# Optimization experiments

Measured on AMD Instinct MI355X. Metric: run time of the kernel, lower is better.

Reference implementation:

```python
import jax, jax.numpy as jnp
import numpy as np

RGB_W = (0.2989, 0.587, 0.114)
EPS = 1e-8  # guard only; original divides without eps


def _saliency_map(img):
    """Faithful jax port of SaliencyMap: gray -> uint8 -> cv2.Sobel(ksize=3,
    BORDER_REFLECT_101) -> magnitude -> per-image min-max normalize.
    img: [B, C, H, W] float in [0,1]. Returns [B, 1, H, W] float32.
    """
    B, C, H, W = img.shape
    if C == 3:
        gray = RGB_W[0] * img[:, 0] + RGB_W[1] * img[:, 1] + RGB_W[2] * img[:, 2]
    else:
        gray = img[:, 0]
    # (gray*255).astype(np.uint8): truncating cast, then cv2 promotes to float
    q = (gray * 255.0).astype(jnp.uint8).astype(jnp.float32)  # [B,H,W]
    # cv2 default border: BORDER_REFLECT_101 == jnp.pad mode 'reflect'
    p = jnp.pad(q, ((0, 0), (1, 1), (1, 1)), mode='reflect')  # [B,H+2,W+2]
    # Sobel x (correlation with [[-1,0,1],[-2,0,2],[-1,0,1]])
    gx = (p[:, :-2, 2:] + 2.0 * p[:, 1:-1, 2:] + p[:, 2:, 2:]
          - p[:, :-2, :-2] - 2.0 * p[:, 1:-1, :-2] - p[:, 2:, :-2])
    # Sobel y (transpose kernel)
    gy = (p[:, 2:, :-2] + 2.0 * p[:, 2:, 1:-1] + p[:, 2:, 2:]
          - p[:, :-2, :-2] - 2.0 * p[:, :-2, 1:-1] - p[:, :-2, 2:])
    mag = jnp.sqrt(gx * gx + gy * gy)  # [B,H,W]
    mn = jnp.min(mag, axis=(1, 2), keepdims=True)
    mx = jnp.max(mag, axis=(1, 2), keepdims=True)
    norm = (mag - mn) / jnp.maximum(mx - mn, EPS)  # cv2 NORM_MINMAX to [0,1]
    return norm[:, None]  # [B,1,H,W]


def setup_inputs() -> dict:
    key = jax.random.key(0)
    k1, k2, k3 = jax.random.split(key, 3)
    shape = (16, 3, 512, 512)
    return {
        "img_vis": jax.random.uniform(k1, shape, dtype=jnp.float32),
        "img_ir": jax.random.uniform(k2, shape, dtype=jnp.float32),
        "img_fusion": jax.random.uniform(k3, shape, dtype=jnp.float32),
    }


def reference(img_vis, img_ir, img_fusion):
    s_vis = _saliency_map(img_vis)  # [B,1,H,W]
    s_ir = _saliency_map(img_ir)
    denom = s_vis + s_ir + EPS  # eps guard against 0/0 (see notes)
    w_vis = s_vis / denom
    w_ir = s_ir / denom
    img_sal = w_vis * img_vis + w_ir * img_ir  # broadcasts over channels
    loss = jnp.mean(jnp.abs(img_sal - img_fusion))  # F.l1_loss (mean)
    return loss
```

## Files before the change

kernel.cpp:

```cpp
#include <hip/hip_runtime.h>
#include <hip/hip_bf16.h>
#include <stdint.h>

#define H 512
#define W 512
#define HW (H * W)
#define NSTRIP 128

__device__ __forceinline__ int refl(int i, int n) {
    return i < 0 ? -i : (i >= n ? 2 * n - 2 - i : i);
}

__device__ __forceinline__ uint2 gray8(float4 ra, float4 rb, float4 ga, float4 gb,
                                       float4 ba, float4 bb) {
    uint32_t t0 = (uint32_t)((0.2989f * ra.x + 0.587f * ga.x + 0.114f * ba.x) * 255.0f);
    uint32_t t1 = (uint32_t)((0.2989f * ra.y + 0.587f * ga.y + 0.114f * ba.y) * 255.0f);
    uint32_t t2 = (uint32_t)((0.2989f * ra.z + 0.587f * ga.z + 0.114f * ba.z) * 255.0f);
    uint32_t t3 = (uint32_t)((0.2989f * ra.w + 0.587f * ga.w + 0.114f * ba.w) * 255.0f);
    uint32_t t4 = (uint32_t)((0.2989f * rb.x + 0.587f * gb.x + 0.114f * bb.x) * 255.0f);
    uint32_t t5 = (uint32_t)((0.2989f * rb.y + 0.587f * gb.y + 0.114f * bb.y) * 255.0f);
    uint32_t t6 = (uint32_t)((0.2989f * rb.z + 0.587f * gb.z + 0.114f * bb.z) * 255.0f);
    uint32_t t7 = (uint32_t)((0.2989f * rb.w + 0.587f * gb.w + 0.114f * bb.w) * 255.0f);
    uint2 o;
    o.x = t0 | (t1 << 8) | (t2 << 16) | (t3 << 24);
    o.y = t4 | (t5 << 8) | (t6 << 16) | (t7 << 24);
    return o;
}

__global__ __launch_bounds__(256) void k_gray(const float* __restrict__ vis,
                                              const float* __restrict__ ir,
                                              uint8_t* __restrict__ qvis,
                                              uint8_t* __restrict__ qir, int B) {
    int lane = threadIdx.x & 63;
    int gwave = blockIdx.x * 4 + (threadIdx.x >> 6);
    int per_src = B * 256;
    int src = gwave >= per_src;
    int rem = src ? gwave - per_src : gwave;
    int b  = rem >> 8;
    int y0 = (rem & 255) * 2;

    const float4* p4 = (const float4*)((src ? ir : vis) + (size_t)b * 3 * HW);
    uint8_t* q = (src ? qir : qvis) + (size_t)b * HW;

    int o0 = y0 * (W / 4) + lane * 2;
    int o1 = o0 + (W / 4);
    float4 r0a = p4[o0],                 r0b = p4[o0 + 1];
    float4 g0a = p4[o0 + HW / 4],        g0b = p4[o0 + 1 + HW / 4];
    float4 b0a = p4[o0 + 2 * (HW / 4)],  b0b = p4[o0 + 1 + 2 * (HW / 4)];
    float4 r1a = p4[o1],                 r1b = p4[o1 + 1];
    float4 g1a = p4[o1 + HW / 4],        g1b = p4[o1 + 1 + HW / 4];
    float4 b1a = p4[o1 + 2 * (HW / 4)],  b1b = p4[o1 + 1 + 2 * (HW / 4)];

    uint2 q0 = gray8(r0a, r0b, g0a, g0b, b0a, b0b);
    uint2 q1 = gray8(r1a, r1b, g1a, g1b, b1a, b1b);
    *(uint2*)(q + (size_t)y0 * W + lane * 8)       = q0;
    *(uint2*)(q + (size_t)(y0 + 1) * W + lane * 8) = q1;
}

__device__ __forceinline__ void row_cols(uint2 v, int lane, float* __restrict__ c) {
    uint32_t lx = __shfl_up(v.y, 1);
    uint32_t rx = __shfl_down(v.x, 1);
    uint32_t lb = (lane == 0)  ? ((v.x >> 8) & 0xffu)  : (lx >> 24);
    uint32_t rb = (lane == 63) ? ((v.y >> 16) & 0xffu) : (rx & 0xffu);
    c[0] = (float)lb;
    c[1] = (float)(v.x & 0xffu);
    c[2] = (float)((v.x >> 8) & 0xffu);
    c[3] = (float)((v.x >> 16) & 0xffu);
    c[4] = (float)(v.x >> 24);
    c[5] = (float)(v.y & 0xffu);
    c[6] = (float)((v.y >> 8) & 0xffu);
    c[7] = (float)((v.y >> 16) & 0xffu);
    c[8] = (float)(v.y >> 24);
    c[9] = (float)rb;
}

__device__ __forceinline__ void sobel_row8(const uint8_t* __restrict__ q, int y, int lane,
                                           float* __restrict__ mag) {
    const uint2* rm = (const uint2*)(q + (size_t)refl(y - 1, H) * W);
    const uint2* r0 = (const uint2*)(q + (size_t)y * W);
    const uint2* rp = (const uint2*)(q + (size_t)refl(y + 1, H) * W);
    uint2 vm = rm[lane], v0 = r0[lane], vp = rp[lane];
    float c0[10], c1[10], c2[10];
    row_cols(vm, lane, c0);
    row_cols(v0, lane, c1);
    row_cols(vp, lane, c2);
    float sx[10], sy[10];
    #pragma unroll
    for (int j = 0; j < 10; ++j) {
        sx[j] = c0[j] + 2.0f * c1[j] + c2[j];
        sy[j] = c2[j] - c0[j];
    }
    #pragma unroll
    for (int k = 0; k < 8; ++k) {
        float gx = sx[k + 2] - sx[k];
        float gy = sy[k] + 2.0f * sy[k + 1] + sy[k + 2];
        mag[k] = sqrtf(gx * gx + gy * gy);
    }
}

__global__ __launch_bounds__(256) void k_mm(const uint8_t* __restrict__ qvis,
                                            const uint8_t* __restrict__ qir,
                                            float* __restrict__ pm, int B) {
    int lane = threadIdx.x & 63;
    int gwave = blockIdx.x * 4 + (threadIdx.x >> 6);
    int per_src = B * NSTRIP;
    int src = gwave >= per_src;
    int rem = src ? gwave - per_src : gwave;
    int b     = rem >> 7;
    int strip = rem & 127;
    int y0 = strip * 4;
    const uint8_t* q = (src ? qir : qvis) + (size_t)b * HW;

    float mn = INFINITY, mx = 0.0f;
    #pragma unroll
    for (int r = 0; r < 4; ++r) {
        float mag[8];
        sobel_row8(q, y0 + r, lane, mag);
        #pragma unroll
        for (int k = 0; k < 8; ++k) {
            mn = fminf(mn, mag[k]);
            mx = fmaxf(mx, mag[k]);
        }
    }
    #pragma unroll
    for (int o = 32; o > 0; o >>= 1) {
        mn = fminf(mn, __shfl_down(mn, o));
        mx = fmaxf(mx, __shfl_down(mx, o));
    }
    if (lane == 0) {
        float* o = pm + ((size_t)(src * B + b) * NSTRIP + strip) * 2;
        o[0] = mn;
        o[1] = mx;
    }
}

__global__ __launch_bounds__(256) void k_loss(const float* __restrict__ vis,
                                              const float* __restrict__ ir,
                                              const float* __restrict__ fus,
                                              const uint8_t* __restrict__ qvis,
                                              const uint8_t* __restrict__ qir,
                                              const float* __restrict__ pm,
                                              float* __restrict__ partial, int B) {
    int w = threadIdx.x >> 6, lane = threadIdx.x & 63;
    int b = blockIdx.x >> 6;
    int y0 = (blockIdx.x & 63) * 8;

    __shared__ float sred[4];
    {
        int src = w >> 1, qsel = w & 1;
        const float* base = pm + (size_t)(src * B + b) * NSTRIP * 2;
        float v0 = base[lane * 2 + qsel];
        float v1 = base[(lane + 64) * 2 + qsel];
        float v = qsel ? fmaxf(v0, v1) : fminf(v0, v1);
        if (qsel == 0) {
            #pragma unroll
            for (int o = 32; o > 0; o >>= 1) v = fminf(v, __shfl_down(v, o));
        } else {
            #pragma unroll
            for (int o = 32; o > 0; o >>= 1) v = fmaxf(v, __shfl_down(v, o));
        }
        if (lane == 0) sred[w] = v;
    }
    __syncthreads();
    float mn_v = sred[0], mx_v = sred[1], mn_i = sred[2], mx_i = sred[3];
    float inv_v = 1.0f / fmaxf(mx_v - mn_v, 1e-8f);
    float inv_i = 1.0f / fmaxf(mx_i - mn_i, 1e-8f);

    float acc = 0.0f;
    #pragma unroll
    for (int rr = 0; rr < 2; ++rr) {
        int y = y0 + w + rr * 4;
        float mv[8], mi[8];
        sobel_row8(qvis + (size_t)b * HW, y, lane, mv);
        sobel_row8(qir  + (size_t)b * HW, y, lane, mi);

        float wv[8], wi[8];
        #pragma unroll
        for (int k = 0; k < 8; ++k) {
            float sv = (mv[k] - mn_v) * inv_v;
            float si = (mi[k] - mn_i) * inv_i;
            float den = sv + si + 1e-8f;
            float rden = 1.0f / den;
            wv[k] = sv * rden;
            wi[k] = si * rden;
        }

        int i = y * W + lane * 8;
        #pragma unroll
        for (int ch = 0; ch < 3; ++ch) {
            size_t e4 = ((((size_t)b * 3 + ch) * HW) + i) >> 2;
            const float4* v4 = (const float4*)vis;
            const float4* r4 = (const float4*)ir;
            const float4* f4 = (const float4*)fus;
            float4 va = v4[e4], vb = v4[e4 + 1];
            float4 ra = r4[e4], rb = r4[e4 + 1];
            float4 fa = f4[e4], fb = f4[e4 + 1];
            acc += fabsf(wv[0] * va.x + wi[0] * ra.x - fa.x);
            acc += fabsf(wv[1] * va.y + wi[1] * ra.y - fa.y);
            acc += fabsf(wv[2] * va.z + wi[2] * ra.z - fa.z);
            acc += fabsf(wv[3] * va.w + wi[3] * ra.w - fa.w);
            acc += fabsf(wv[4] * vb.x + wi[4] * rb.x - fb.x);
            acc += fabsf(wv[5] * vb.y + wi[5] * rb.y - fb.y);
            acc += fabsf(wv[6] * vb.z + wi[6] * rb.z - fb.z);
            acc += fabsf(wv[7] * vb.w + wi[7] * rb.w - fb.w);
        }
    }

    #pragma unroll
    for (int o = 32; o > 0; o >>= 1) acc += __shfl_down(acc, o);
    __shared__ float ssum[4];
    if (lane == 0) ssum[w] = acc;
    __syncthreads();
    if (threadIdx.x == 0) partial[blockIdx.x] = ssum[0] + ssum[1] + ssum[2] + ssum[3];
}

__global__ void k_final(const float* __restrict__ partial, int n, float* __restrict__ out,
                        long long N) {
    double s = 0.0;
    for (int i = threadIdx.x; i < n; i += 256) s += (double)partial[i];
    __shared__ double sm[256];
    sm[threadIdx.x] = s;
    __syncthreads();
    for (int k = 128; k > 0; k >>= 1) {
        if (threadIdx.x < k) sm[threadIdx.x] += sm[threadIdx.x + k];
        __syncthreads();
    }
    if (threadIdx.x == 0) out[0] = (float)(sm[0] / (double)N);
}

extern "C" void kernel_launch(void* const* d_in, const int* in_sizes, int n_in,
                              void* d_out, int out_size, void* d_ws, size_t ws_size,
                              hipStream_t stream) {
    const float* vis = (const float*)d_in[0];
    const float* ir  = (const float*)d_in[1];
    const float* fus = (const float*)d_in[2];
    int B = in_sizes[0] / (3 * HW);

    uint8_t* qvis = (uint8_t*)d_ws;
    uint8_t* qir  = qvis + (size_t)B * HW;
    float* pm      = (float*)(qir + (size_t)B * HW);
    float* partial = pm + (size_t)2 * B * NSTRIP * 2;
    float* out = (float*)d_out;

    int nblk_gray = 2 * B * 256 / 4;
    k_gray<<<nblk_gray, 256, 0, stream>>>(vis, ir, qvis, qir, B);

    int nblk_mm = 2 * B * NSTRIP / 4;
    k_mm<<<nblk_mm, 256, 0, stream>>>(qvis, qir, pm, B);

    int nblk_loss = B * (H / 8);
    k_loss<<<nblk_loss, 256, 0, stream>>>(vis, ir, fus, qvis, qir, pm, partial, B);

    k_final<<<1, 256, 0, stream>>>(partial, nblk_loss, out, (long long)B * 3 * HW);
}
```

Baseline: 58.65 us.

## Fuse grayscale quantization into Sobel kernels and drop uint8 intermediate

```diff
diff --git a/kernel.cpp b/kernel.cpp
--- a/kernel.cpp
+++ b/kernel.cpp
@@ -11,84 +11,46 @@
     return i < 0 ? -i : (i >= n ? 2 * n - 2 - i : i);
 }
 
-__device__ __forceinline__ uint2 gray8(float4 ra, float4 rb, float4 ga, float4 gb,
-                                       float4 ba, float4 bb) {
-    uint32_t t0 = (uint32_t)((0.2989f * ra.x + 0.587f * ga.x + 0.114f * ba.x) * 255.0f);
-    uint32_t t1 = (uint32_t)((0.2989f * ra.y + 0.587f * ga.y + 0.114f * ba.y) * 255.0f);
-    uint32_t t2 = (uint32_t)((0.2989f * ra.z + 0.587f * ga.z + 0.114f * ba.z) * 255.0f);
-    uint32_t t3 = (uint32_t)((0.2989f * ra.w + 0.587f * ga.w + 0.114f * ba.w) * 255.0f);
-    uint32_t t4 = (uint32_t)((0.2989f * rb.x + 0.587f * gb.x + 0.114f * bb.x) * 255.0f);
-    uint32_t t5 = (uint32_t)((0.2989f * rb.y + 0.587f * gb.y + 0.114f * bb.y) * 255.0f);
-    uint32_t t6 = (uint32_t)((0.2989f * rb.z + 0.587f * gb.z + 0.114f * bb.z) * 255.0f);
-    uint32_t t7 = (uint32_t)((0.2989f * rb.w + 0.587f * gb.w + 0.114f * bb.w) * 255.0f);
-    uint2 o;
-    o.x = t0 | (t1 << 8) | (t2 << 16) | (t3 << 24);
-    o.y = t4 | (t5 << 8) | (t6 << 16) | (t7 << 24);
-    return o;
-}
-
-__global__ __launch_bounds__(256) void k_gray(const float* __restrict__ vis,
-                                              const float* __restrict__ ir,
-                                              uint8_t* __restrict__ qvis,
-                                              uint8_t* __restrict__ qir, int B) {
-    int lane = threadIdx.x & 63;
-    int gwave = blockIdx.x * 4 + (threadIdx.x >> 6);
-    int per_src = B * 256;
-    int src = gwave >= per_src;
-    int rem = src ? gwave - per_src : gwave;
-    int b  = rem >> 8;
-    int y0 = (rem & 255) * 2;
-
-    const float4* p4 = (const float4*)((src ? ir : vis) + (size_t)b * 3 * HW);
-    uint8_t* q = (src ? qir : qvis) + (size_t)b * HW;
-
-    int o0 = y0 * (W / 4) + lane * 2;
-    int o1 = o0 + (W / 4);
-    float4 r0a = p4[o0],                 r0b = p4[o0 + 1];
-    float4 g0a = p4[o0 + HW / 4],        g0b = p4[o0 + 1 + HW / 4];
-    float4 b0a = p4[o0 + 2 * (HW / 4)],  b0b = p4[o0 + 1 + 2 * (HW / 4)];
-    float4 r1a = p4[o1],                 r1b = p4[o1 + 1];
-    float4 g1a = p4[o1 + HW / 4],        g1b = p4[o1 + 1 + HW / 4];
-    float4 b1a = p4[o1 + 2 * (HW / 4)],  b1b = p4[o1 + 1 + 2 * (HW / 4)];
-
-    uint2 q0 = gray8(r0a, r0b, g0a, g0b, b0a, b0b);
-    uint2 q1 = gray8(r1a, r1b, g1a, g1b, b1a, b1b);
-    *(uint2*)(q + (size_t)y0 * W + lane * 8)       = q0;
-    *(uint2*)(q + (size_t)(y0 + 1) * W + lane * 8) = q1;
-}
-
-__device__ __forceinline__ void row_cols(uint2 v, int lane, float* __restrict__ c) {
-    uint32_t lx = __shfl_up(v.y, 1);
-    uint32_t rx = __shfl_down(v.x, 1);
-    uint32_t lb = (lane == 0)  ? ((v.x >> 8) & 0xffu)  : (lx >> 24);
-    uint32_t rb = (lane == 63) ? ((v.y >> 16) & 0xffu) : (rx & 0xffu);
-    c[0] = (float)lb;
-    c[1] = (float)(v.x & 0xffu);
-    c[2] = (float)((v.x >> 8) & 0xffu);
-    c[3] = (float)((v.x >> 16) & 0xffu);
-    c[4] = (float)(v.x >> 24);
-    c[5] = (float)(v.y & 0xffu);
-    c[6] = (float)((v.y >> 8) & 0xffu);
-    c[7] = (float)((v.y >> 16) & 0xffu);
-    c[8] = (float)(v.y >> 24);
-    c[9] = (float)rb;
-}
-
-__device__ __forceinline__ void sobel_row8(const uint8_t* __restrict__ q, int y, int lane,
-                                           float* __restrict__ mag) {
-    const uint2* rm = (const uint2*)(q + (size_t)refl(y - 1, H) * W);
-    const uint2* r0 = (const uint2*)(q + (size_t)y * W);
-    const uint2* rp = (const uint2*)(q + (size_t)refl(y + 1, H) * W);
-    uint2 vm = rm[lane], v0 = r0[lane], vp = rp[lane];
-    float c0[10], c1[10], c2[10];
-    row_cols(vm, lane, c0);
-    row_cols(v0, lane, c1);
-    row_cols(vp, lane, c2);
+__device__ __forceinline__ void gray8f(float4 ra, float4 rb, float4 ga, float4 gb,
+                                       float4 ba, float4 bb, float* __restrict__ g) {
+    g[0] = floorf((0.2989f * ra.x + 0.587f * ga.x + 0.114f * ba.x) * 255.0f);
+    g[1] = floorf((0.2989f * ra.y + 0.587f * ga.y + 0.114f * ba.y) * 255.0f);
+    g[2] = floorf((0.2989f * ra.z + 0.587f * ga.z + 0.114f * ba.z) * 255.0f);
+    g[3] = floorf((0.2989f * ra.w + 0.587f * ga.w + 0.114f * ba.w) * 255.0f);
+    g[4] = floorf((0.2989f * rb.x + 0.587f * gb.x + 0.114f * bb.x) * 255.0f);
+    g[5] = floorf((0.2989f * rb.y + 0.587f * gb.y + 0.114f * bb.y) * 255.0f);
+    g[6] = floorf((0.2989f * rb.z + 0.587f * gb.z + 0.114f * bb.z) * 255.0f);
+    g[7] = floorf((0.2989f * rb.w + 0.587f * gb.w + 0.114f * bb.w) * 255.0f);
+}
+
+__device__ __forceinline__ void grayrow(const float4* __restrict__ p4, int row, int lane,
+                                        float* __restrict__ g) {
+    int o = row * (W / 4) + lane * 2;
+    float4 ra = p4[o],                 rb = p4[o + 1];
+    float4 ga = p4[o + HW / 4],        gb = p4[o + 1 + HW / 4];
+    float4 ba = p4[o + 2 * (HW / 4)],  bb = p4[o + 1 + 2 * (HW / 4)];
+    gray8f(ra, rb, ga, gb, ba, bb, g);
+}
+
+__device__ __forceinline__ void win10(const float* __restrict__ g, int lane,
+                                      float* __restrict__ h) {
+    #pragma unroll
+    for (int j = 0; j < 8; ++j) h[j + 1] = g[j];
+    float up = __shfl_up(g[7], 1);
+    float dn = __shfl_down(g[0], 1);
+    h[0] = (lane == 0)  ? g[1] : up;
+    h[9] = (lane == 63) ? g[6] : dn;
+}
+
+__device__ __forceinline__ void sobel8(const float* __restrict__ hm,
+                                       const float* __restrict__ h0,
+                                       const float* __restrict__ hp,
+                                       float* __restrict__ mag) {
     float sx[10], sy[10];
     #pragma unroll
     for (int j = 0; j < 10; ++j) {
-        sx[j] = c0[j] + 2.0f * c1[j] + c2[j];
-        sy[j] = c2[j] - c0[j];
+        sx[j] = hm[j] + 2.0f * h0[j] + hp[j];
+        sy[j] = hp[j] - hm[j];
     }
     #pragma unroll
     for (int k = 0; k < 8; ++k) {
@@ -98,24 +60,39 @@
     }
 }
 
-__global__ __launch_bounds__(256) void k_mm(const uint8_t* __restrict__ qvis,
-                                            const uint8_t* __restrict__ qir,
+__device__ __forceinline__ void sobel_rgb(const float4* __restrict__ p4, int y, int lane,
+                                          float* __restrict__ mag) {
+    float gm[8], g0[8], gp[8];
+    grayrow(p4, refl(y - 1, H), lane, gm);
+    grayrow(p4, y,              lane, g0);
+    grayrow(p4, refl(y + 1, H), lane, gp);
+    float hm[10], h0[10], hp[10];
+    win10(gm, lane, hm);
+    win10(g0, lane, h0);
+    win10(gp, lane, hp);
+    sobel8(hm, h0, hp, mag);
+}
+
+__global__ __launch_bounds__(256) void k_mm(const float* __restrict__ vis,
+                                            const float* __restrict__ ir,
                                             float* __restrict__ pm, int B) {
     int lane = threadIdx.x & 63;
-    int gwave = blockIdx.x * 4 + (threadIdx.x >> 6);
+    int nwg = gridDim.x;
+    int bid = (blockIdx.x & 7) * (nwg >> 3) + (blockIdx.x >> 3);
+    int gwave = bid * 4 + (threadIdx.x >> 6);
     int per_src = B * NSTRIP;
     int src = gwave >= per_src;
     int rem = src ? gwave - per_src : gwave;
     int b     = rem >> 7;
     int strip = rem & 127;
     int y0 = strip * 4;
-    const uint8_t* q = (src ? qir : qvis) + (size_t)b * HW;
+    const float4* p4 = (const float4*)((src ? ir : vis) + (size_t)b * 3 * HW);
 
     float mn = INFINITY, mx = 0.0f;
     #pragma unroll
     for (int r = 0; r < 4; ++r) {
         float mag[8];
-        sobel_row8(q, y0 + r, lane, mag);
+        sobel_rgb(p4, y0 + r, lane, mag);
         #pragma unroll
         for (int k = 0; k < 8; ++k) {
             mn = fminf(mn, mag[k]);
@@ -134,16 +111,32 @@
     }
 }
 
+__device__ __forceinline__ float acc8(const float* __restrict__ wv,
+                                      const float* __restrict__ wi,
+                                      float4 va, float4 vb, float4 ra, float4 rb,
+                                      float4 fa, float4 fb) {
+    float s = 0.0f;
+    s += fabsf(wv[0] * va.x + wi[0] * ra.x - fa.x);
+    s += fabsf(wv[1] * va.y + wi[1] * ra.y - fa.y);
+    s += fabsf(wv[2] * va.z + wi[2] * ra.z - fa.z);
+    s += fabsf(wv[3] * va.w + wi[3] * ra.w - fa.w);
+    s += fabsf(wv[4] * vb.x + wi[4] * rb.x - fb.x);
+    s += fabsf(wv[5] * vb.y + wi[5] * rb.y - fb.y);
+    s += fabsf(wv[6] * vb.z + wi[6] * rb.z - fb.z);
+    s += fabsf(wv[7] * vb.w + wi[7] * rb.w - fb.w);
+    return s;
+}
+
 __global__ __launch_bounds__(256) void k_loss(const float* __restrict__ vis,
                                               const float* __restrict__ ir,
                                               const float* __restrict__ fus,
-                                              const uint8_t* __restrict__ qvis,
-                                              const uint8_t* __restrict__ qir,
                                               const float* __restrict__ pm,
                                               float* __restrict__ partial, int B) {
     int w = threadIdx.x >> 6, lane = threadIdx.x & 63;
-    int b = blockIdx.x >> 6;
-    int y0 = (blockIdx.x & 63) * 8;
+    int nwg = gridDim.x;
+    int bid = (blockIdx.x & 7) * (nwg >> 3) + (blockIdx.x >> 3);
+    int b = bid >> 7;
+    int y = (bid & 127) * 4 + w;
 
     __shared__ float sred[4];
     {
@@ -166,48 +159,59 @@
     float inv_v = 1.0f / fmaxf(mx_v - mn_v, 1e-8f);
     float inv_i = 1.0f / fmaxf(mx_i - mn_i, 1e-8f);
 
+    const float4* pv = (const float4*)(vis + (size_t)b * 3 * HW);
+    const float4* pi = (const float4*)(ir  + (size_t)b * 3 * HW);
+    const float4* pf = (const float4*)(fus + (size_t)b * 3 * HW);
+
+    int o = y * (W / 4) + lane * 2;
+    float4 vra = pv[o],                 vrb = pv[o + 1];
+    float4 vga = pv[o + HW / 4],        vgb = pv[o + 1 + HW / 4];
+    float4 vba = pv[o + 2 * (HW / 4)],  vbb = pv[o + 1 + 2 * (HW / 4)];
+    float4 ira = pi[o],                 irb = pi[o + 1];
+    float4 iga = pi[o + HW / 4],        igb = pi[o + 1 + HW / 4];
+    float4 iba = pi[o + 2 * (HW / 4)],  ibb = pi[o + 1 + 2 * (HW / 4)];
+    float4 fra = pf[o],                 frb = pf[o + 1];
+    float4 fga = pf[o + HW / 4],        fgb = pf[o + 1 + HW / 4];
+    float4 fba = pf[o + 2 * (HW / 4)],  fbb = pf[o + 1 + 2 * (HW / 4)];
+
+    float mv[8], mi[8];
+    {
+        float g0[8], gm[8], gp[8];
+        gray8f(vra, vrb, vga, vgb, vba, vbb, g0);
+        grayrow(pv, refl(y - 1, H), lane, gm);
+        grayrow(pv, refl(y + 1, H), lane, gp);
+        float hm[10], h0[10], hp[10];
+        win10(gm, lane, hm); win10(g0, lane, h0); win10(gp, lane, hp);
+        sobel8(hm, h0, hp, mv);
+    }
+    {
+        float g0[8], gm[8], gp[8];
+        gray8f(ira, irb, iga, igb, iba, ibb, g0);
+        grayrow(pi, refl(y - 1, H), lane, gm);
+        grayrow(pi, refl(y + 1, H), lane, gp);
+        float hm[10], h0[10], hp[10];
+        win10(gm, lane, hm); win10(g0, lane, h0); win10(gp, lane, hp);
+        sobel8(hm, h0, hp, mi);
+    }
+
+    float wv[8], wi[8];
+    #pragma unroll
+    for (int k = 0; k < 8; ++k) {
+        float sv = (mv[k] - mn_v) * inv_v;
+        float si = (mi[k] - mn_i) * inv_i;
+        float den = sv + si + 1e-8f;
+        float rden = 1.0f / den;
+        wv[k] = sv * rden;
+        wi[k] = si * rden;
+    }
+
     float acc = 0.0f;
-    #pragma unroll
-    for (int rr = 0; rr < 2; ++rr) {
-        int y = y0 + w + rr * 4;
-        float mv[8], mi[8];
-        sobel_row8(qvis + (size_t)b * HW, y, lane, mv);
-        sobel_row8(qir  + (size_t)b * HW, y, lane, mi);
-
-        float wv[8], wi[8];
-        #pragma unroll
-        for (int k = 0; k < 8; ++k) {
-            float sv = (mv[k] - mn_v) * inv_v;
-            float si = (mi[k] - mn_i) * inv_i;
-            float den = sv + si + 1e-8f;
-            float rden = 1.0f / den;
-            wv[k] = sv * rden;
-            wi[k] = si * rden;
-        }
-
-        int i = y * W + lane * 8;
-        #pragma unroll
-        for (int ch = 0; ch < 3; ++ch) {
-            size_t e4 = ((((size_t)b * 3 + ch) * HW) + i) >> 2;
-            const float4* v4 = (const float4*)vis;
-            const float4* r4 = (const float4*)ir;
-            const float4* f4 = (const float4*)fus;
-            float4 va = v4[e4], vb = v4[e4 + 1];
-            float4 ra = r4[e4], rb = r4[e4 + 1];
-            float4 fa = f4[e4], fb = f4[e4 + 1];
-            acc += fabsf(wv[0] * va.x + wi[0] * ra.x - fa.x);
-            acc += fabsf(wv[1] * va.y + wi[1] * ra.y - fa.y);
-            acc += fabsf(wv[2] * va.z + wi[2] * ra.z - fa.z);
-            acc += fabsf(wv[3] * va.w + wi[3] * ra.w - fa.w);
-            acc += fabsf(wv[4] * vb.x + wi[4] * rb.x - fb.x);
-            acc += fabsf(wv[5] * vb.y + wi[5] * rb.y - fb.y);
-            acc += fabsf(wv[6] * vb.z + wi[6] * rb.z - fb.z);
-            acc += fabsf(wv[7] * vb.w + wi[7] * rb.w - fb.w);
-        }
-    }
-
-    #pragma unroll
-    for (int o = 32; o > 0; o >>= 1) acc += __shfl_down(acc, o);
+    acc += acc8(wv, wi, vra, vrb, ira, irb, fra, frb);
+    acc += acc8(wv, wi, vga, vgb, iga, igb, fga, fgb);
+    acc += acc8(wv, wi, vba, vbb, iba, ibb, fba, fbb);
+
+    #pragma unroll
+    for (int o2 = 32; o2 > 0; o2 >>= 1) acc += __shfl_down(acc, o2);
     __shared__ float ssum[4];
     if (lane == 0) ssum[w] = acc;
     __syncthreads();
@@ -236,20 +240,15 @@
     const float* fus = (const float*)d_in[2];
     int B = in_sizes[0] / (3 * HW);
 
-    uint8_t* qvis = (uint8_t*)d_ws;
-    uint8_t* qir  = qvis + (size_t)B * HW;
-    float* pm      = (float*)(qir + (size_t)B * HW);
+    float* pm      = (float*)d_ws;
     float* partial = pm + (size_t)2 * B * NSTRIP * 2;
     float* out = (float*)d_out;
 
-    int nblk_gray = 2 * B * 256 / 4;
-    k_gray<<<nblk_gray, 256, 0, stream>>>(vis, ir, qvis, qir, B);
-
     int nblk_mm = 2 * B * NSTRIP / 4;
-    k_mm<<<nblk_mm, 256, 0, stream>>>(qvis, qir, pm, B);
-
-    int nblk_loss = B * (H / 8);
-    k_loss<<<nblk_loss, 256, 0, stream>>>(vis, ir, fus, qvis, qir, pm, partial, B);
+    k_mm<<<nblk_mm, 256, 0, stream>>>(vis, ir, pm, B);
+
+    int nblk_loss = B * H / 4;
+    k_loss<<<nblk_loss, 256, 0, stream>>>(vis, ir, fus, pm, partial, B);
 
     k_final<<<1, 256, 0, stream>>>(partial, nblk_loss, out, (long long)B * 3 * HW);
 }
```

Result: slower. 70.94 us (+21.0%).
